# Optimization experiments

Hardware: AMD Instinct MI355X
Metric: run time of the kernel (lower is better)

The kernel has to match this reference:

```python
import jax, jax.numpy as jnp
import numpy as np

HIDDEN = 4096
INTER = 11008
GROUPSIZE = 128
PACK = 8


def dequant_gptq(qweight, scales, zeros, groupsize):
    """Dequantize GPTQ 4-bit packed weights.
    qweight: [K//8, N] int32 (8 nibbles along K), scales: [G, N] fp16,
    zeros: [G, N//8] int32 (8 nibbles along N). Returns [K, N] float32:
    w[k,n] = q[k,n]*s[g,n] - (z[g,n]+1)*s[g,n],  g = k // groupsize.
    """
    K = qweight.shape[0] * PACK
    N = qweight.shape[1]
    k = jnp.arange(K)
    # unpack along K: [K, N]
    q = (qweight[k // PACK, :] >> ((k % PACK) * 4)[:, None]) & 15
    n = jnp.arange(N)
    # unpack zero-points along N: [G, N]
    z = (zeros[:, n // PACK] >> ((n % PACK) * 4)[None, :]) & 15
    s = scales.astype(jnp.float32)                       # [G, N]
    zp = (z.astype(jnp.float32) + 1.0) * s               # [G, N]
    g = k // groupsize
    return q.astype(jnp.float32) * s[g] - zp[g]          # [K, N]


def setup_inputs() -> dict:
    key = jax.random.key(0)
    ks = jax.random.split(key, 11)
    imax = 2147483647
    G_h = HIDDEN // GROUPSIZE      # 32
    G_i = (INTER + GROUPSIZE - 1) // GROUPSIZE  # 86
    x = (jax.random.normal(ks[0], (2, 2048, HIDDEN), dtype=jnp.float32) * 0.5).astype(jnp.float16)
    return {
        "x": x,
        "gate_qweight": jax.random.randint(ks[1], (HIDDEN // PACK, INTER), 0, imax, dtype=jnp.int32),
        "gate_scales": (jax.random.uniform(ks[2], (G_h, INTER), dtype=jnp.float32) * 0.01 + 0.001).astype(jnp.float16),
        "gate_zeros": jax.random.randint(ks[3], (G_h, INTER // PACK), 0, imax, dtype=jnp.int32),
        "up_qweight": jax.random.randint(ks[4], (HIDDEN // PACK, INTER), 0, imax, dtype=jnp.int32),
        "up_scales": (jax.random.uniform(ks[5], (G_h, INTER), dtype=jnp.float32) * 0.01 + 0.001).astype(jnp.float16),
        "up_zeros": jax.random.randint(ks[6], (G_h, INTER // PACK), 0, imax, dtype=jnp.int32),
        "down_qweight": jax.random.randint(ks[7], (INTER // PACK, HIDDEN), 0, imax, dtype=jnp.int32),
        "down_scales": (jax.random.uniform(ks[8], (G_i, HIDDEN), dtype=jnp.float32) * 0.01 + 0.001).astype(jnp.float16),
        "down_zeros": jax.random.randint(ks[9], (G_i, HIDDEN // PACK), 0, imax, dtype=jnp.int32),
    }


def reference(x, gate_qweight, gate_scales, gate_zeros,
              up_qweight, up_scales, up_zeros,
              down_qweight, down_scales, down_zeros):
    B, S, H = x.shape
    x2 = x.reshape(-1, H).astype(jnp.float32)            # [M, H]
    Wg = dequant_gptq(gate_qweight, gate_scales, gate_zeros, GROUPSIZE)  # [H, I]
    Wu = dequant_gptq(up_qweight, up_scales, up_zeros, GROUPSIZE)        # [H, I]
    Wd = dequant_gptq(down_qweight, down_scales, down_zeros, GROUPSIZE)  # [I, H]
    gate = x2 @ Wg                                       # [M, I] fp32 accumulate
    up = x2 @ Wu                                         # [M, I]
    inter = gate * jax.nn.sigmoid(gate) * up             # SiLU(gate) * up
    out = (inter @ Wd).astype(jnp.float16)               # [M, H]
    return out.reshape(B, S, H)
```

## Files before the change

### kernel.cpp

```cpp
#include <hip/hip_runtime.h>
#include <stdint.h>


#define HIDDEN 4096
#define INTER  11008
#define BM 256
#define BN 256
#define BK 64

typedef __bf16 bf16x8 __attribute__((ext_vector_type(8)));
typedef float f32x4 __attribute__((ext_vector_type(4)));

__device__ __forceinline__ ushort f2bf_rne(float f) {
  uint32_t u = __float_as_uint(f);
  u += 0x7FFFu + ((u >> 16) & 1u);
  return (ushort)(u >> 16);
}

__device__ __forceinline__ float bf2f(ushort h) {
  return __uint_as_float(((uint32_t)h) << 16);
}

__global__ void f32_to_bf16_kernel(const float* __restrict__ src,
                                   ushort* __restrict__ dst, int n4) {
  const int i = blockIdx.x * 256 + threadIdx.x;
  if (i < n4) {
    const float4 v = ((const float4*)src)[i];
    ushort4 o;
    o.x = f2bf_rne(v.x); o.y = f2bf_rne(v.y);
    o.z = f2bf_rne(v.z); o.w = f2bf_rne(v.w);
    ((ushort4*)dst)[i] = o;
  }
}

__global__ void dequant_kernel(const int32_t* __restrict__ qw,
                               const float* __restrict__ sc,
                               const int32_t* __restrict__ zr,
                               ushort* __restrict__ Bp,
                               int Nfull, int n0, int nc) {
  const int n_local = blockIdx.x * 128 + threadIdx.x;
  const int k8 = blockIdx.y;
  const int n = n0 + n_local;
  const int g = k8 >> 4;
  const uint32_t q = (uint32_t)qw[(size_t)k8 * Nfull + n];
  const float s = sc[(size_t)g * Nfull + n];
  const uint32_t zv = (uint32_t)zr[(size_t)g * (Nfull >> 3) + (n >> 3)];
  const int z1 = (int)((zv >> ((n & 7) * 4)) & 15u) + 1;
  union { ushort h[8]; uint4 v; } o;
#pragma unroll
  for (int j = 0; j < 8; j++) {
    const int qi = (int)((q >> (4 * j)) & 15u) - z1;
    o.h[j] = f2bf_rne((float)qi * s);
  }
  *(uint4*)(Bp + ((size_t)k8 * nc + n_local) * 8) = o.v;
}

#define GL_LDS(gp, lp)                                                        \
  __builtin_amdgcn_global_load_lds(                                           \
      (const __attribute__((address_space(1))) uint32_t*)(gp),                \
      (__attribute__((address_space(3))) uint32_t*)(lp), 16, 0, 0)
#define BAR()  do { __builtin_amdgcn_s_barrier(); asm volatile("" ::: "memory"); } while (0)
#define WVM4() asm volatile("s_waitcnt vmcnt(4)" ::: "memory")
#define WVM0() asm volatile("s_waitcnt vmcnt(0)" ::: "memory")
#define WLG0() asm volatile("s_waitcnt lgkmcnt(0)" ::: "memory")

template <int MODE>
__launch_bounds__(512, 2)
__global__ void gemm_bt_kernel(const ushort* __restrict__ A,
                               const ushort* __restrict__ Bp,
                               void* __restrict__ Cv,
                               int K, int nc, int lda, int ldc) {
  __shared__ ushort sAs[2][BM * BK];
  __shared__ ushort sBs[2][(BK / 8) * BN * 8];

  const int tid = threadIdx.x;
  const int w = tid >> 6;
  const int lane = tid & 63;
  const int l16 = lane & 15;
  const int quad = lane >> 4;
  const int wm16 = (w >> 2) * 16;
  const int wn = (w & 3) * 64;

  const int gx = gridDim.x;
  const int nwg = gx * (int)gridDim.y;
  const int orig = blockIdx.y * gx + blockIdx.x;
  const int q8 = nwg >> 3, r8 = nwg & 7;
  const int xcd = orig & 7, sidx = orig >> 3;
  const int wg = (xcd < r8 ? xcd * (q8 + 1) : r8 * (q8 + 1) + (xcd - r8) * q8) + sidx;
  const int m0 = (wg / gx) * BM;
  const int bn0 = (wg % gx) * BN;

  const int arow = tid >> 3;
  const int apk8 = ((tid & 7) ^ (arow & 7)) * 8;
  const int bpr = tid >> 8;
  const int bcol = tid & 255;
  const ushort* aSrc = A + (size_t)(m0 + arow) * lda + apk8;
  const ushort* bSrc = Bp + ((size_t)bpr * nc + bn0 + bcol) * 8;

  f32x4 acc[8][4];
#pragma unroll
  for (int a = 0; a < 8; a++)
#pragma unroll
    for (int j = 0; j < 4; j++) acc[a][j] = (f32x4){0.f, 0.f, 0.f, 0.f};

  const int NT = K / BK;

#define STAGE_A(r, buf, kt) \
  GL_LDS(aSrc + (size_t)(r) * 64 * lda + (kt), (buf) + (r) * 4096 + w * 512)
#define STAGE_B(r, buf, kp) \
  GL_LDS(bSrc + ((kp) + (size_t)(r) * 2) * (size_t)nc * 8, (buf) + (r) * 4096 + w * 512)

  {
    ushort* sAn = sAs[0];
    ushort* sBn = sBs[0];
    STAGE_A(0, sAn, (size_t)0); STAGE_A(1, sAn, (size_t)0);
    STAGE_B(0, sBn, (size_t)0); STAGE_B(1, sBn, (size_t)0);
    STAGE_A(2, sAn, (size_t)0); STAGE_A(3, sAn, (size_t)0);
    STAGE_B(2, sBn, (size_t)0); STAGE_B(3, sBn, (size_t)0);
  }

#pragma unroll 1
  for (int t = 0; t < NT; ++t) {
    const ushort* sAc = sAs[t & 1];
    const ushort* sBc = sBs[t & 1];
    ushort* sAn = sAs[(t & 1) ^ 1];
    ushort* sBn = sBs[(t & 1) ^ 1];
    const int tn = (t + 1 < NT) ? t + 1 : t;
    const size_t ktn = (size_t)tn * BK;
    const size_t kpn = (size_t)tn * 8;

    WVM4(); BAR();

    bf16x8 af[4], bf[4];
    const ushort* pA0 = sAc + (size_t)(wm16 + l16) * 64 + ((quad ^ (l16 & 7)) * 8);
    const ushort* pA1 = sAc + (size_t)(wm16 + l16) * 64 + (((4 ^ quad) ^ (l16 & 7)) * 8);
    const ushort* pB0 = sBc + ((size_t)(quad * 256) + wn + l16) * 8;
    const ushort* pB1 = sBc + ((size_t)((4 + quad) * 256) + wn + l16) * 8;

#pragma unroll
    for (int i = 0; i < 4; i++) af[i] = *(const bf16x8*)(pA0 + i * 2048);
#pragma unroll
    for (int j = 0; j < 4; j++) bf[j] = *(const bf16x8*)(pB0 + j * 128);
    STAGE_A(0, sAn, ktn); STAGE_A(1, sAn, ktn);
    BAR(); WLG0();
    __builtin_amdgcn_s_setprio(1);
#pragma unroll
    for (int i = 0; i < 4; i++)
#pragma unroll
      for (int j = 0; j < 4; j++)
        acc[i][j] = __builtin_amdgcn_mfma_f32_16x16x32_bf16(af[i], bf[j], acc[i][j], 0, 0, 0);
    __builtin_amdgcn_s_setprio(0);
    WVM4();
    BAR();

#pragma unroll
    for (int i = 0; i < 4; i++) af[i] = *(const bf16x8*)(pA0 + 128 * 64 + i * 2048);
    STAGE_B(0, sBn, kpn); STAGE_B(1, sBn, kpn);
    BAR(); WLG0();
    __builtin_amdgcn_s_setprio(1);
#pragma unroll
    for (int i = 0; i < 4; i++)
#pragma unroll
      for (int j = 0; j < 4; j++)
        acc[4 + i][j] = __builtin_amdgcn_mfma_f32_16x16x32_bf16(af[i], bf[j], acc[4 + i][j], 0, 0, 0);
    __builtin_amdgcn_s_setprio(0);
    WVM4();
    BAR();

#pragma unroll
    for (int i = 0; i < 4; i++) af[i] = *(const bf16x8*)(pA1 + i * 2048);
#pragma unroll
    for (int j = 0; j < 4; j++) bf[j] = *(const bf16x8*)(pB1 + j * 128);
    STAGE_A(2, sAn, ktn); STAGE_A(3, sAn, ktn);
    BAR(); WLG0();
    __builtin_amdgcn_s_setprio(1);
#pragma unroll
    for (int i = 0; i < 4; i++)
#pragma unroll
      for (int j = 0; j < 4; j++)
        acc[i][j] = __builtin_amdgcn_mfma_f32_16x16x32_bf16(af[i], bf[j], acc[i][j], 0, 0, 0);
    __builtin_amdgcn_s_setprio(0);
    BAR();

#pragma unroll
    for (int i = 0; i < 4; i++) af[i] = *(const bf16x8*)(pA1 + 128 * 64 + i * 2048);
    STAGE_B(2, sBn, kpn); STAGE_B(3, sBn, kpn);
    BAR(); WLG0();
    __builtin_amdgcn_s_setprio(1);
#pragma unroll
    for (int i = 0; i < 4; i++)
#pragma unroll
      for (int j = 0; j < 4; j++)
        acc[4 + i][j] = __builtin_amdgcn_mfma_f32_16x16x32_bf16(af[i], bf[j], acc[4 + i][j], 0, 0, 0);
    __builtin_amdgcn_s_setprio(0);
  }
  WVM0();

#pragma unroll
  for (int a = 0; a < 8; a++) {
    const int gmb = m0 + (a >> 2) * 128 + (a & 3) * 32 + wm16 + quad * 4;
#pragma unroll
    for (int r = 0; r < 4; r++) {
      const int gm = gmb + r;
      if (MODE == 2) {
        float* crow = (float*)Cv + (size_t)gm * ldc + bn0 + wn;
#pragma unroll
        for (int j = 0; j < 4; j++) crow[j * 16 + l16] = acc[a][j][r];
      } else {
        ushort* crow = (ushort*)Cv + (size_t)gm * ldc + bn0 + wn;
#pragma unroll
        for (int j = 0; j < 4; j++) {
          float v = acc[a][j][r];
          if (MODE == 1) {
            const float gv = bf2f(crow[j * 16 + l16]);
            v = (gv / (1.0f + __expf(-gv))) * v;
          }
          crow[j * 16 + l16] = f2bf_rne(v);
        }
      }
    }
  }
}

extern "C" void kernel_launch(void* const* d_in, const int* in_sizes, int n_in,
                              void* d_out, int out_size, void* d_ws, size_t ws_size,
                              hipStream_t stream) {
  (void)n_in; (void)out_size;
  const float*   x   = (const float*)d_in[0];
  const int32_t* gq  = (const int32_t*)d_in[1];
  const float*   gs  = (const float*)d_in[2];
  const int32_t* gz  = (const int32_t*)d_in[3];
  const int32_t* uq  = (const int32_t*)d_in[4];
  const float*   us  = (const float*)d_in[5];
  const int32_t* uz  = (const int32_t*)d_in[6];
  const int32_t* dq  = (const int32_t*)d_in[7];
  const float*   dsc = (const float*)d_in[8];
  const int32_t* dz  = (const int32_t*)d_in[9];
  float* outp = (float*)d_out;

  const int M = in_sizes[0] / HIDDEN;

  const size_t W = ws_size;
  const size_t col12 = (size_t)HIDDEN * 2;
  const size_t col3  = (size_t)INTER * 2;
  const size_t xb_bytes = (size_t)M * HIDDEN * 2;
  int MC = 256;
  for (int cand = M; cand >= 256; cand >>= 1) {
    if (xb_bytes + (size_t)cand * INTER * 2 + col3 * 256 <= W) { MC = cand; break; }
  }
  ushort* xb = (ushort*)d_ws;
  ushort* gi = xb + (size_t)M * HIDDEN;
  ushort* wb = gi + (size_t)MC * INTER;
  const size_t used = xb_bytes + (size_t)MC * INTER * 2;
  const size_t wbuf = (W > used) ? W - used : 0;
  int NC12 = (int)(wbuf / col12); NC12 &= ~255;
  if (NC12 < 256) NC12 = 256;
  if (NC12 > INTER) NC12 = INTER;
  int NC3 = (int)(wbuf / col3); NC3 &= ~255;
  if (NC3 < 256) NC3 = 256;
  if (NC3 > HIDDEN) NC3 = HIDDEN;

  const int n4 = M * HIDDEN / 4;
  f32_to_bf16_kernel<<<(n4 + 255) / 256, 256, 0, stream>>>(x, xb, n4);

  for (int m0 = 0; m0 < M; m0 += MC) {
    const ushort* xm = xb + (size_t)m0 * HIDDEN;
    for (int n0 = 0; n0 < INTER; ) {
      int nc = INTER - n0; if (nc > NC12) nc = NC12;
      dequant_kernel<<<dim3(nc / 128, HIDDEN / 8), 128, 0, stream>>>(
          gq, gs, gz, wb, INTER, n0, nc);
      gemm_bt_kernel<0><<<dim3(nc / BN, MC / BM), 512, 0, stream>>>(
          xm, wb, gi + n0, HIDDEN, nc, HIDDEN, INTER);
      n0 += nc;
    }
    for (int n0 = 0; n0 < INTER; ) {
      int nc = INTER - n0; if (nc > NC12) nc = NC12;
      dequant_kernel<<<dim3(nc / 128, HIDDEN / 8), 128, 0, stream>>>(
          uq, us, uz, wb, INTER, n0, nc);
      gemm_bt_kernel<1><<<dim3(nc / BN, MC / BM), 512, 0, stream>>>(
          xm, wb, gi + n0, HIDDEN, nc, HIDDEN, INTER);
      n0 += nc;
    }
    for (int n0 = 0; n0 < HIDDEN; ) {
      int nc = HIDDEN - n0; if (nc > NC3) nc = NC3;
      dequant_kernel<<<dim3(nc / 128, INTER / 8), 128, 0, stream>>>(
          dq, dsc, dz, wb, HIDDEN, n0, nc);
      gemm_bt_kernel<2><<<dim3(nc / BN, MC / BM), 512, 0, stream>>>(
          gi, wb, (void*)(outp + (size_t)m0 * HIDDEN + n0), INTER, nc, INTER, HIDDEN);
      n0 += nc;
    }
  }
}
```

Measured before the change: 1.165 ms.

## Double-buffer register fragments to overlap LDS reads with MFMA in GEMM main loop

Restructures the GEMM main loop so the next phase's A/B fragments are read from LDS into a second register set while the current MFMA block runs. The first fragments of the next tile are prefetched at the end of each iteration, and waits are relaxed from vmcnt(4) to vmcnt(2) with fewer barriers. sched_barrier fences stop the compiler from reordering loads around the MFMA blocks. This is meant to hide LDS latency behind tensor-core work, at the cost of more fragment registers and a trickier ordering of barriers and waitcnts, which could race on the buffers.

```diff
diff --git a/kernel.cpp b/kernel.cpp
--- a/kernel.cpp
+++ b/kernel.cpp
@@ -61,8 +61,10 @@
       (__attribute__((address_space(3))) uint32_t*)(lp), 16, 0, 0)
 #define BAR()  do { __builtin_amdgcn_s_barrier(); asm volatile("" ::: "memory"); } while (0)
 #define WVM4() asm volatile("s_waitcnt vmcnt(4)" ::: "memory")
+#define WVM2() asm volatile("s_waitcnt vmcnt(2)" ::: "memory")
 #define WVM0() asm volatile("s_waitcnt vmcnt(0)" ::: "memory")
 #define WLG0() asm volatile("s_waitcnt lgkmcnt(0)" ::: "memory")
+#define SCHED0() __builtin_amdgcn_sched_barrier(0)
 
 template <int MODE>
 __launch_bounds__(512, 2)
@@ -80,6 +82,7 @@
   const int quad = lane >> 4;
   const int wm16 = (w >> 2) * 16;
   const int wn = (w & 3) * 64;
+  const int swz = l16 & 7;
 
   const int gx = gridDim.x;
   const int nwg = gx * (int)gridDim.y;
@@ -103,6 +106,8 @@
 #pragma unroll
     for (int j = 0; j < 4; j++) acc[a][j] = (f32x4){0.f, 0.f, 0.f, 0.f};
 
+  bf16x8 afs0[4], afs1[4], bfs0[4], bfs1[4];
+
   const int NT = K / BK;
 
 #define STAGE_A(r, buf, kt) \
@@ -111,12 +116,21 @@
   GL_LDS(bSrc + ((kp) + (size_t)(r) * 2) * (size_t)nc * 8, (buf) + (r) * 4096 + w * 512)
 
   {
-    ushort* sAn = sAs[0];
-    ushort* sBn = sBs[0];
-    STAGE_A(0, sAn, (size_t)0); STAGE_A(1, sAn, (size_t)0);
-    STAGE_B(0, sBn, (size_t)0); STAGE_B(1, sBn, (size_t)0);
-    STAGE_A(2, sAn, (size_t)0); STAGE_A(3, sAn, (size_t)0);
-    STAGE_B(2, sBn, (size_t)0); STAGE_B(3, sBn, (size_t)0);
+    ushort* sA0 = sAs[0];
+    ushort* sB0 = sBs[0];
+    STAGE_A(0, sA0, (size_t)0); STAGE_A(1, sA0, (size_t)0);
+    STAGE_B(0, sB0, (size_t)0); STAGE_B(1, sB0, (size_t)0);
+    STAGE_A(2, sA0, (size_t)0); STAGE_A(3, sA0, (size_t)0);
+    STAGE_B(2, sB0, (size_t)0); STAGE_B(3, sB0, (size_t)0);
+    WVM4();
+    BAR();
+    const ushort* a0 = sA0 + (size_t)(wm16 + l16) * 64;
+#pragma unroll
+    for (int i = 0; i < 4; i++)
+      afs0[i] = *(const bf16x8*)(a0 + i * 2048 + ((quad ^ swz) * 8));
+#pragma unroll
+    for (int j = 0; j < 4; j++)
+      bfs0[j] = *(const bf16x8*)(sB0 + ((size_t)(quad * 256) + wn + j * 16 + l16) * 8);
   }
 
 #pragma unroll 1
@@ -128,70 +142,75 @@
     const int tn = (t + 1 < NT) ? t + 1 : t;
     const size_t ktn = (size_t)tn * BK;
     const size_t kpn = (size_t)tn * 8;
-
-    WVM4(); BAR();
-
-    bf16x8 af[4], bf[4];
-    const ushort* pA0 = sAc + (size_t)(wm16 + l16) * 64 + ((quad ^ (l16 & 7)) * 8);
-    const ushort* pA1 = sAc + (size_t)(wm16 + l16) * 64 + (((4 ^ quad) ^ (l16 & 7)) * 8);
-    const ushort* pB0 = sBc + ((size_t)(quad * 256) + wn + l16) * 8;
-    const ushort* pB1 = sBc + ((size_t)((4 + quad) * 256) + wn + l16) * 8;
-
-#pragma unroll
-    for (int i = 0; i < 4; i++) af[i] = *(const bf16x8*)(pA0 + i * 2048);
-#pragma unroll
-    for (int j = 0; j < 4; j++) bf[j] = *(const bf16x8*)(pB0 + j * 128);
+    const ushort* aLo = sAc + (size_t)(wm16 + l16) * 64;
+    const ushort* aHi = aLo + 128 * 64;
+
+    WVM2();
+    BAR(); WLG0(); SCHED0();
+#pragma unroll
+    for (int i = 0; i < 4; i++)
+      afs1[i] = *(const bf16x8*)(aHi + i * 2048 + ((quad ^ swz) * 8));
     STAGE_A(0, sAn, ktn); STAGE_A(1, sAn, ktn);
-    BAR(); WLG0();
+    SCHED0();
     __builtin_amdgcn_s_setprio(1);
 #pragma unroll
     for (int i = 0; i < 4; i++)
 #pragma unroll
       for (int j = 0; j < 4; j++)
-        acc[i][j] = __builtin_amdgcn_mfma_f32_16x16x32_bf16(af[i], bf[j], acc[i][j], 0, 0, 0);
+        acc[i][j] = __builtin_amdgcn_mfma_f32_16x16x32_bf16(afs0[i], bfs0[j], acc[i][j], 0, 0, 0);
     __builtin_amdgcn_s_setprio(0);
-    WVM4();
-    BAR();
-
-#pragma unroll
-    for (int i = 0; i < 4; i++) af[i] = *(const bf16x8*)(pA0 + 128 * 64 + i * 2048);
+
+    WVM2();
+    BAR(); WLG0(); SCHED0();
+#pragma unroll
+    for (int i = 0; i < 4; i++)
+      afs0[i] = *(const bf16x8*)(aLo + i * 2048 + (((4 ^ quad) ^ swz) * 8));
+#pragma unroll
+    for (int j = 0; j < 4; j++)
+      bfs1[j] = *(const bf16x8*)(sBc + ((size_t)((4 + quad) * 256) + wn + j * 16 + l16) * 8);
     STAGE_B(0, sBn, kpn); STAGE_B(1, sBn, kpn);
-    BAR(); WLG0();
+    SCHED0();
     __builtin_amdgcn_s_setprio(1);
 #pragma unroll
     for (int i = 0; i < 4; i++)
 #pragma unroll
       for (int j = 0; j < 4; j++)
-        acc[4 + i][j] = __builtin_amdgcn_mfma_f32_16x16x32_bf16(af[i], bf[j], acc[4 + i][j], 0, 0, 0);
+        acc[4 + i][j] = __builtin_amdgcn_mfma_f32_16x16x32_bf16(afs1[i], bfs0[j], acc[4 + i][j], 0, 0, 0);
     __builtin_amdgcn_s_setprio(0);
-    WVM4();
-    BAR();
-
-#pragma unroll
-    for (int i = 0; i < 4; i++) af[i] = *(const bf16x8*)(pA1 + i * 2048);
-#pragma unroll
-    for (int j = 0; j < 4; j++) bf[j] = *(const bf16x8*)(pB1 + j * 128);
+
+    BAR(); WLG0(); SCHED0();
+#pragma unroll
+    for (int i = 0; i < 4; i++)
+      afs1[i] = *(const bf16x8*)(aHi + i * 2048 + (((4 ^ quad) ^ swz) * 8));
     STAGE_A(2, sAn, ktn); STAGE_A(3, sAn, ktn);
-    BAR(); WLG0();
+    SCHED0();
     __builtin_amdgcn_s_setprio(1);
 #pragma unroll
     for (int i = 0; i < 4; i++)
 #pragma unroll
       for (int j = 0; j < 4; j++)
-        acc[i][j] = __builtin_amdgcn_mfma_f32_16x16x32_bf16(af[i], bf[j], acc[i][j], 0, 0, 0);
+        acc[i][j] = __builtin_amdgcn_mfma_f32_16x16x32_bf16(afs0[i], bfs1[j], acc[i][j], 0, 0, 0);
     __builtin_amdgcn_s_setprio(0);
-    BAR();
-
-#pragma unroll
-    for (int i = 0; i < 4; i++) af[i] = *(const bf16x8*)(pA1 + 128 * 64 + i * 2048);
+
+    WVM2();
+    BAR(); WLG0(); SCHED0();
+    {
+      const ushort* aNx = sAn + (size_t)(wm16 + l16) * 64;
+#pragma unroll
+      for (int i = 0; i < 4; i++)
+        afs0[i] = *(const bf16x8*)(aNx + i * 2048 + ((quad ^ swz) * 8));
+#pragma unroll
+      for (int j = 0; j < 4; j++)
+        bfs0[j] = *(const bf16x8*)(sBn + ((size_t)(quad * 256) + wn + j * 16 + l16) * 8);
+    }
     STAGE_B(2, sBn, kpn); STAGE_B(3, sBn, kpn);
-    BAR(); WLG0();
+    SCHED0();
     __builtin_amdgcn_s_setprio(1);
 #pragma unroll
     for (int i = 0; i < 4; i++)
 #pragma unroll
       for (int j = 0; j < 4; j++)
-        acc[4 + i][j] = __builtin_amdgcn_mfma_f32_16x16x32_bf16(af[i], bf[j], acc[4 + i][j], 0, 0, 0);
+        acc[4 + i][j] = __builtin_amdgcn_mfma_f32_16x16x32_bf16(afs1[i], bfs1[j], acc[4 + i][j], 0, 0, 0);
     __builtin_amdgcn_s_setprio(0);
   }
   WVM0();
```

Result: slower. 1.383 ms (+18.7%).

## Restructure GEMM main loop into quadrant-based 8-phase ping-pong schedule

Applied to the files above, without the earlier changes.

Replaces the 4-phase per-K-tile loop with a two-tile unrolled loop. Each 8-wave block now owns a contiguous 128x64 quadrant per wave, split into 2x2 subtiles, and issues interleaved LDS reads, MFMA and global-to-LDS staging with fewer lgkmcnt waits and a vmcnt(6) depth. The intent is to keep loads in flight longer and improve A/B fragment reuse across MFMA clusters, reducing stalls at barriers. The cost is more register pressure from extra fragment buffers and a more intricate staging order that assumes NT is even.

```diff
diff --git a/kernel.cpp b/kernel.cpp
--- a/kernel.cpp
+++ b/kernel.cpp
@@ -60,9 +60,8 @@
       (const __attribute__((address_space(1))) uint32_t*)(gp),                \
       (__attribute__((address_space(3))) uint32_t*)(lp), 16, 0, 0)
 #define BAR()  do { __builtin_amdgcn_s_barrier(); asm volatile("" ::: "memory"); } while (0)
-#define WVM4() asm volatile("s_waitcnt vmcnt(4)" ::: "memory")
+#define WVM6() asm volatile("s_waitcnt vmcnt(6)" ::: "memory")
 #define WVM0() asm volatile("s_waitcnt vmcnt(0)" ::: "memory")
-#define WLG0() asm volatile("s_waitcnt lgkmcnt(0)" ::: "memory")
 
 template <int MODE>
 __launch_bounds__(512, 2)
@@ -70,16 +69,19 @@
                                const ushort* __restrict__ Bp,
                                void* __restrict__ Cv,
                                int K, int nc, int lda, int ldc) {
-  __shared__ ushort sAs[2][BM * BK];
-  __shared__ ushort sBs[2][(BK / 8) * BN * 8];
+  __shared__ ushort sA0[BM * BK];
+  __shared__ ushort sB0[(BK / 8) * BN * 8];
+  __shared__ ushort sA1[BM * BK];
+  __shared__ ushort sB1[(BK / 8) * BN * 8];
 
   const int tid = threadIdx.x;
   const int w = tid >> 6;
   const int lane = tid & 63;
   const int l16 = lane & 15;
   const int quad = lane >> 4;
-  const int wm16 = (w >> 2) * 16;
-  const int wn = (w & 3) * 64;
+  const int wm = w >> 2;
+  const int wn = w & 3;
+  const int swz = l16 & 7;
 
   const int gx = gridDim.x;
   const int nwg = gx * (int)gridDim.y;
@@ -97,125 +99,145 @@
   const ushort* aSrc = A + (size_t)(m0 + arow) * lda + apk8;
   const ushort* bSrc = Bp + ((size_t)bpr * nc + bn0 + bcol) * 8;
 
-  f32x4 acc[8][4];
-#pragma unroll
-  for (int a = 0; a < 8; a++)
-#pragma unroll
-    for (int j = 0; j < 4; j++) acc[a][j] = (f32x4){0.f, 0.f, 0.f, 0.f};
+  f32x4 acc[2][2][4][2];
+#pragma unroll
+  for (int rh = 0; rh < 2; rh++)
+#pragma unroll
+    for (int ch = 0; ch < 2; ch++)
+#pragma unroll
+      for (int i = 0; i < 4; i++)
+#pragma unroll
+        for (int jj = 0; jj < 2; jj++)
+          acc[rh][ch][i][jj] = (f32x4){0.f, 0.f, 0.f, 0.f};
+
+  bf16x8 afr[4][2], bA[2][2], bB[2][2];
 
   const int NT = K / BK;
-
-#define STAGE_A(r, buf, kt) \
-  GL_LDS(aSrc + (size_t)(r) * 64 * lda + (kt), (buf) + (r) * 4096 + w * 512)
-#define STAGE_B(r, buf, kp) \
-  GL_LDS(bSrc + ((kp) + (size_t)(r) * 2) * (size_t)nc * 8, (buf) + (r) * 4096 + w * 512)
-
-  {
-    ushort* sAn = sAs[0];
-    ushort* sBn = sBs[0];
-    STAGE_A(0, sAn, (size_t)0); STAGE_A(1, sAn, (size_t)0);
-    STAGE_B(0, sBn, (size_t)0); STAGE_B(1, sBn, (size_t)0);
-    STAGE_A(2, sAn, (size_t)0); STAGE_A(3, sAn, (size_t)0);
-    STAGE_B(2, sBn, (size_t)0); STAGE_B(3, sBn, (size_t)0);
-  }
+  const int NI = NT >> 1;
+
+#define SA(r, s, buf) \
+  GL_LDS(aSrc + (size_t)(r) * 64 * lda + (size_t)(s) * BK, (buf) + (r) * 4096 + w * 512)
+#define SB(r, s, buf) \
+  GL_LDS(bSrc + ((size_t)(s) * 8 + (r) * 2) * (size_t)nc * 8, (buf) + (r) * 4096 + w * 512)
+
+#define RD_A(sbuf, rh)                                                         \
+  do {                                                                         \
+    const ushort* _a = (sbuf) + ((size_t)(wm * 128 + (rh) * 64 + l16)) * 64;   \
+    _Pragma("unroll") for (int i = 0; i < 4; i++) {                            \
+      afr[i][0] = *(const bf16x8*)(_a + i * 1024 + ((quad ^ swz) * 8));        \
+      afr[i][1] = *(const bf16x8*)(_a + i * 1024 + (((quad + 4) ^ swz) * 8));  \
+    }                                                                          \
+  } while (0)
+#define RD_B(sbuf, ch, dst)                                                    \
+  do {                                                                         \
+    const int _c = wn * 64 + (ch) * 32 + l16;                                  \
+    _Pragma("unroll") for (int jj = 0; jj < 2; jj++) {                         \
+      dst[jj][0] = *(const bf16x8*)((sbuf) + ((quad * 256) + _c + jj * 16) * 8);       \
+      dst[jj][1] = *(const bf16x8*)((sbuf) + (((quad + 4) * 256) + _c + jj * 16) * 8); \
+    }                                                                          \
+  } while (0)
+#define MM(rh, ch, bset)                                                       \
+  do {                                                                         \
+    __builtin_amdgcn_s_setprio(1);                                             \
+    _Pragma("unroll") for (int kk = 0; kk < 2; kk++)                           \
+    _Pragma("unroll") for (int i = 0; i < 4; i++)                              \
+    _Pragma("unroll") for (int jj = 0; jj < 2; jj++)                           \
+      acc[rh][ch][i][jj] = __builtin_amdgcn_mfma_f32_16x16x32_bf16(            \
+          afr[i][kk], bset[jj][kk], acc[rh][ch][i][jj], 0, 0, 0);              \
+    __builtin_amdgcn_s_setprio(0);                                             \
+  } while (0)
+
+  SA(0, 0, sA0); SA(2, 0, sA0);
+  SB(0, 0, sB0); SB(1, 0, sB0); SB(2, 0, sB0); SB(3, 0, sB0);
+  SA(1, 0, sA0); SA(3, 0, sA0);
+  SA(0, 1, sA1); SA(2, 1, sA1);
+  SB(0, 1, sB1); SB(1, 1, sB1); SB(2, 1, sB1); SB(3, 1, sB1);
+  WVM6();
+  BAR();
 
 #pragma unroll 1
-  for (int t = 0; t < NT; ++t) {
-    const ushort* sAc = sAs[t & 1];
-    const ushort* sBc = sBs[t & 1];
-    ushort* sAn = sAs[(t & 1) ^ 1];
-    ushort* sBn = sBs[(t & 1) ^ 1];
-    const int tn = (t + 1 < NT) ? t + 1 : t;
-    const size_t ktn = (size_t)tn * BK;
-    const size_t kpn = (size_t)tn * 8;
-
-    WVM4(); BAR();
-
-    bf16x8 af[4], bf[4];
-    const ushort* pA0 = sAc + (size_t)(wm16 + l16) * 64 + ((quad ^ (l16 & 7)) * 8);
-    const ushort* pA1 = sAc + (size_t)(wm16 + l16) * 64 + (((4 ^ quad) ^ (l16 & 7)) * 8);
-    const ushort* pB0 = sBc + ((size_t)(quad * 256) + wn + l16) * 8;
-    const ushort* pB1 = sBc + ((size_t)((4 + quad) * 256) + wn + l16) * 8;
-
-#pragma unroll
-    for (int i = 0; i < 4; i++) af[i] = *(const bf16x8*)(pA0 + i * 2048);
-#pragma unroll
-    for (int j = 0; j < 4; j++) bf[j] = *(const bf16x8*)(pB0 + j * 128);
-    STAGE_A(0, sAn, ktn); STAGE_A(1, sAn, ktn);
-    BAR(); WLG0();
-    __builtin_amdgcn_s_setprio(1);
-#pragma unroll
-    for (int i = 0; i < 4; i++)
-#pragma unroll
-      for (int j = 0; j < 4; j++)
-        acc[i][j] = __builtin_amdgcn_mfma_f32_16x16x32_bf16(af[i], bf[j], acc[i][j], 0, 0, 0);
-    __builtin_amdgcn_s_setprio(0);
-    WVM4();
-    BAR();
-
-#pragma unroll
-    for (int i = 0; i < 4; i++) af[i] = *(const bf16x8*)(pA0 + 128 * 64 + i * 2048);
-    STAGE_B(0, sBn, kpn); STAGE_B(1, sBn, kpn);
-    BAR(); WLG0();
-    __builtin_amdgcn_s_setprio(1);
-#pragma unroll
-    for (int i = 0; i < 4; i++)
-#pragma unroll
-      for (int j = 0; j < 4; j++)
-        acc[4 + i][j] = __builtin_amdgcn_mfma_f32_16x16x32_bf16(af[i], bf[j], acc[4 + i][j], 0, 0, 0);
-    __builtin_amdgcn_s_setprio(0);
-    WVM4();
-    BAR();
-
-#pragma unroll
-    for (int i = 0; i < 4; i++) af[i] = *(const bf16x8*)(pA1 + i * 2048);
-#pragma unroll
-    for (int j = 0; j < 4; j++) bf[j] = *(const bf16x8*)(pB1 + j * 128);
-    STAGE_A(2, sAn, ktn); STAGE_A(3, sAn, ktn);
-    BAR(); WLG0();
-    __builtin_amdgcn_s_setprio(1);
-#pragma unroll
-    for (int i = 0; i < 4; i++)
-#pragma unroll
-      for (int j = 0; j < 4; j++)
-        acc[i][j] = __builtin_amdgcn_mfma_f32_16x16x32_bf16(af[i], bf[j], acc[i][j], 0, 0, 0);
-    __builtin_amdgcn_s_setprio(0);
-    BAR();
-
-#pragma unroll
-    for (int i = 0; i < 4; i++) af[i] = *(const bf16x8*)(pA1 + 128 * 64 + i * 2048);
-    STAGE_B(2, sBn, kpn); STAGE_B(3, sBn, kpn);
-    BAR(); WLG0();
-    __builtin_amdgcn_s_setprio(1);
-#pragma unroll
-    for (int i = 0; i < 4; i++)
-#pragma unroll
-      for (int j = 0; j < 4; j++)
-        acc[4 + i][j] = __builtin_amdgcn_mfma_f32_16x16x32_bf16(af[i], bf[j], acc[4 + i][j], 0, 0, 0);
-    __builtin_amdgcn_s_setprio(0);
+  for (int it = 0; it < NI; ++it) {
+    const int c1 = 2 * it + 1;
+    const int s2 = (2 * it + 2 < NT) ? 2 * it + 2 : NT - 2;
+    const int s3 = (2 * it + 3 < NT) ? 2 * it + 3 : NT - 1;
+
+    RD_A(sA0, 0); RD_B(sB0, 0, bA);
+    SA(1, c1, sA1); SA(3, c1, sA1);
+    BAR();
+    MM(0, 0, bA);
+    BAR();
+    RD_B(sB0, 1, bB);
+    SA(0, s2, sA0); SA(2, s2, sA0);
+    BAR();
+    MM(0, 1, bB);
+    BAR();
+    RD_A(sA0, 1);
+    SB(0, s2, sB0); SB(1, s2, sB0);
+    BAR();
+    MM(1, 0, bA);
+    BAR();
+    SB(2, s2, sB0); SB(3, s2, sB0);
+    BAR();
+    MM(1, 1, bB);
+    WVM6();
+    BAR();
+    RD_A(sA1, 0); RD_B(sB1, 0, bA);
+    SA(1, s2, sA0); SA(3, s2, sA0);
+    BAR();
+    MM(0, 0, bA);
+    BAR();
+    RD_B(sB1, 1, bB);
+    SA(0, s3, sA1); SA(2, s3, sA1);
+    BAR();
+    MM(0, 1, bB);
+    BAR();
+    RD_A(sA1, 1);
+    SB(0, s3, sB1); SB(1, s3, sB1);
+    BAR();
+    MM(1, 0, bA);
+    BAR();
+    SB(2, s3, sB1); SB(3, s3, sB1);
+    BAR();
+    MM(1, 1, bB);
+    WVM6();
+    BAR();
   }
   WVM0();
 
-#pragma unroll
-  for (int a = 0; a < 8; a++) {
-    const int gmb = m0 + (a >> 2) * 128 + (a & 3) * 32 + wm16 + quad * 4;
-#pragma unroll
-    for (int r = 0; r < 4; r++) {
-      const int gm = gmb + r;
-      if (MODE == 2) {
-        float* crow = (float*)Cv + (size_t)gm * ldc + bn0 + wn;
-#pragma unroll
-        for (int j = 0; j < 4; j++) crow[j * 16 + l16] = acc[a][j][r];
-      } else {
-        ushort* crow = (ushort*)Cv + (size_t)gm * ldc + bn0 + wn;
-#pragma unroll
-        for (int j = 0; j < 4; j++) {
-          float v = acc[a][j][r];
-          if (MODE == 1) {
-            const float gv = bf2f(crow[j * 16 + l16]);
-            v = (gv / (1.0f + __expf(-gv))) * v;
-          }
-          crow[j * 16 + l16] = f2bf_rne(v);
+#undef SA
+#undef SB
+#undef RD_A
+#undef RD_B
+#undef MM
+
+#pragma unroll
+  for (int rh = 0; rh < 2; rh++) {
+#pragma unroll
+    for (int i = 0; i < 4; i++) {
+#pragma unroll
+      for (int r = 0; r < 4; r++) {
+        const int gm = m0 + wm * 128 + rh * 64 + i * 16 + quad * 4 + r;
+        if (MODE == 2) {
+          float* crow = (float*)Cv + (size_t)gm * ldc + bn0 + wn * 64;
+#pragma unroll
+          for (int ch = 0; ch < 2; ch++)
+#pragma unroll
+            for (int jj = 0; jj < 2; jj++)
+              crow[ch * 32 + jj * 16 + l16] = acc[rh][ch][i][jj][r];
+        } else {
+          ushort* crow = (ushort*)Cv + (size_t)gm * ldc + bn0 + wn * 64;
+#pragma unroll
+          for (int ch = 0; ch < 2; ch++)
+#pragma unroll
+            for (int jj = 0; jj < 2; jj++) {
+              float v = acc[rh][ch][i][jj][r];
+              const int cn = ch * 32 + jj * 16 + l16;
+              if (MODE == 1) {
+                const float gv = bf2f(crow[cn]);
+                v = (gv / (1.0f + __expf(-gv))) * v;
+              }
+              crow[cn] = f2bf_rne(v);
+            }
         }
       }
     }
```

Result: slower. 1.373 ms (+17.8%).

## Fuse GPTQ dequantization into GEMM B-tile staging, dropping separate dequant pass

Applied to the files above, without the earlier changes.

Removes the standalone dequant kernel and the bf16 weight buffer. Each GEMM workgroup now loads packed int4 weights, scales and zeros straight into registers, expands them to bf16 with packed converts and FMA, and writes them to LDS inside the pipelined main loop. This avoids writing and re-reading the full dequantized weights in global memory and the extra launches. In exchange, every M-block redoes the dequant arithmetic and the B loads become synchronous register loads rather than async global-to-LDS copies, which could stall the MFMA pipeline.

```diff
diff --git a/kernel.cpp b/kernel.cpp
--- a/kernel.cpp
+++ b/kernel.cpp
@@ -33,28 +33,6 @@
   }
 }
 
-__global__ void dequant_kernel(const int32_t* __restrict__ qw,
-                               const float* __restrict__ sc,
-                               const int32_t* __restrict__ zr,
-                               ushort* __restrict__ Bp,
-                               int Nfull, int n0, int nc) {
-  const int n_local = blockIdx.x * 128 + threadIdx.x;
-  const int k8 = blockIdx.y;
-  const int n = n0 + n_local;
-  const int g = k8 >> 4;
-  const uint32_t q = (uint32_t)qw[(size_t)k8 * Nfull + n];
-  const float s = sc[(size_t)g * Nfull + n];
-  const uint32_t zv = (uint32_t)zr[(size_t)g * (Nfull >> 3) + (n >> 3)];
-  const int z1 = (int)((zv >> ((n & 7) * 4)) & 15u) + 1;
-  union { ushort h[8]; uint4 v; } o;
-#pragma unroll
-  for (int j = 0; j < 8; j++) {
-    const int qi = (int)((q >> (4 * j)) & 15u) - z1;
-    o.h[j] = f2bf_rne((float)qi * s);
-  }
-  *(uint4*)(Bp + ((size_t)k8 * nc + n_local) * 8) = o.v;
-}
-
 #define GL_LDS(gp, lp)                                                        \
   __builtin_amdgcn_global_load_lds(                                           \
       (const __attribute__((address_space(1))) uint32_t*)(gp),                \
@@ -64,12 +42,34 @@
 #define WVM0() asm volatile("s_waitcnt vmcnt(0)" ::: "memory")
 #define WLG0() asm volatile("s_waitcnt lgkmcnt(0)" ::: "memory")
 
+__device__ __forceinline__ uint4 expand_packet(uint32_t v, float s, float nz1s) {
+  const uint32_t lo = v & 0x0F0F0F0Fu;
+  const uint32_t hi = (v >> 4) & 0x0F0F0F0Fu;
+  uint4 o;
+  float a0, a1;
+  a0 = fmaf((float)(lo & 0xFFu), s, nz1s);
+  a1 = fmaf((float)(hi & 0xFFu), s, nz1s);
+  asm("v_cvt_pk_bf16_f32 %0, %1, %2" : "=v"(o.x) : "v"(a0), "v"(a1));
+  a0 = fmaf((float)((lo >> 8) & 0xFFu), s, nz1s);
+  a1 = fmaf((float)((hi >> 8) & 0xFFu), s, nz1s);
+  asm("v_cvt_pk_bf16_f32 %0, %1, %2" : "=v"(o.y) : "v"(a0), "v"(a1));
+  a0 = fmaf((float)((lo >> 16) & 0xFFu), s, nz1s);
+  a1 = fmaf((float)((hi >> 16) & 0xFFu), s, nz1s);
+  asm("v_cvt_pk_bf16_f32 %0, %1, %2" : "=v"(o.z) : "v"(a0), "v"(a1));
+  a0 = fmaf((float)(lo >> 24), s, nz1s);
+  a1 = fmaf((float)(hi >> 24), s, nz1s);
+  asm("v_cvt_pk_bf16_f32 %0, %1, %2" : "=v"(o.w) : "v"(a0), "v"(a1));
+  return o;
+}
+
 template <int MODE>
 __launch_bounds__(512, 2)
-__global__ void gemm_bt_kernel(const ushort* __restrict__ A,
-                               const ushort* __restrict__ Bp,
-                               void* __restrict__ Cv,
-                               int K, int nc, int lda, int ldc) {
+__global__ void gemm_fused_kernel(const ushort* __restrict__ A,
+                                  const int32_t* __restrict__ qw,
+                                  const float* __restrict__ sc,
+                                  const int32_t* __restrict__ zr,
+                                  void* __restrict__ Cv,
+                                  int K, int Nfull, int lda, int ldc) {
   __shared__ ushort sAs[2][BM * BK];
   __shared__ ushort sBs[2][(BK / 8) * BN * 8];
 
@@ -80,6 +80,7 @@
   const int quad = lane >> 4;
   const int wm16 = (w >> 2) * 16;
   const int wn = (w & 3) * 64;
+  const int swz = l16 & 7;
 
   const int gx = gridDim.x;
   const int nwg = gx * (int)gridDim.y;
@@ -92,10 +93,14 @@
 
   const int arow = tid >> 3;
   const int apk8 = ((tid & 7) ^ (arow & 7)) * 8;
-  const int bpr = tid >> 8;
+  const ushort* aSrc = A + (size_t)(m0 + arow) * lda + apk8;
+
   const int bcol = tid & 255;
-  const ushort* aSrc = A + (size_t)(m0 + arow) * lda + apk8;
-  const ushort* bSrc = Bp + ((size_t)bpr * nc + bn0 + bcol) * 8;
+  const int prg = tid >> 8;
+  const int32_t* qcol = qw + bn0 + bcol;
+  const float* scol = sc + bn0 + bcol;
+  const int32_t* zcol = zr + ((bn0 + bcol) >> 3);
+  const int zsh = (bcol & 7) * 4;
 
   f32x4 acc[8][4];
 #pragma unroll
@@ -107,19 +112,47 @@
 
 #define STAGE_A(r, buf, kt) \
   GL_LDS(aSrc + (size_t)(r) * 64 * lda + (kt), (buf) + (r) * 4096 + w * 512)
-#define STAGE_B(r, buf, kp) \
-  GL_LDS(bSrc + ((kp) + (size_t)(r) * 2) * (size_t)nc * 8, (buf) + (r) * 4096 + w * 512)
-
-  {
-    ushort* sAn = sAs[0];
-    ushort* sBn = sBs[0];
-    STAGE_A(0, sAn, (size_t)0); STAGE_A(1, sAn, (size_t)0);
-    STAGE_B(0, sBn, (size_t)0); STAGE_B(1, sBn, (size_t)0);
-    STAGE_A(2, sAn, (size_t)0); STAGE_A(3, sAn, (size_t)0);
-    STAGE_B(2, sBn, (size_t)0); STAGE_B(3, sBn, (size_t)0);
-  }
-
-#pragma unroll 1
+
+  uint32_t b4[4]; float sNx; uint32_t zNx;
+#define LOADB(s)                                                   \
+  do {                                                             \
+    const size_t rb = (size_t)(s) * 8 + prg;                       \
+    b4[0] = (uint32_t)qcol[(rb + 0) * (size_t)Nfull];              \
+    b4[1] = (uint32_t)qcol[(rb + 2) * (size_t)Nfull];              \
+    b4[2] = (uint32_t)qcol[(rb + 4) * (size_t)Nfull];              \
+    b4[3] = (uint32_t)qcol[(rb + 6) * (size_t)Nfull];              \
+    sNx = scol[(size_t)((s) >> 1) * Nfull];                        \
+    zNx = (uint32_t)zcol[(size_t)((s) >> 1) * (Nfull >> 3)];       \
+  } while (0)
+
+#define EXPB(buf)                                                        \
+  do {                                                                   \
+    const int z1 = (int)((zNx >> zsh) & 15u) + 1;                        \
+    const float nz = -((float)z1 * sNx);                                 \
+    _Pragma("unroll") for (int r = 0; r < 4; r++) {                      \
+      const uint4 pk = expand_packet(b4[r], sNx, nz);                    \
+      *(uint4*)((buf) + ((size_t)(prg + 2 * r) * 256 + bcol) * 8) = pk;  \
+    }                                                                    \
+  } while (0)
+
+#define MM16(base)                                                       \
+  do {                                                                   \
+    __builtin_amdgcn_s_setprio(1);                                       \
+    _Pragma("unroll") for (int i = 0; i < 4; i++)                        \
+    _Pragma("unroll") for (int j = 0; j < 4; j++)                        \
+      acc[(base) + i][j] = __builtin_amdgcn_mfma_f32_16x16x32_bf16(      \
+          af[i], bf[j], acc[(base) + i][j], 0, 0, 0);                    \
+    __builtin_amdgcn_s_setprio(0);                                       \
+  } while (0)
+
+  LOADB(0);
+  STAGE_A(0, sAs[0], (size_t)0); STAGE_A(1, sAs[0], (size_t)0);
+  STAGE_A(2, sAs[0], (size_t)0); STAGE_A(3, sAs[0], (size_t)0);
+  WVM4();
+  EXPB(sBs[0]);
+  WVM0(); WLG0();
+  BAR();
+
   for (int t = 0; t < NT; ++t) {
     const ushort* sAc = sAs[t & 1];
     const ushort* sBc = sBs[t & 1];
@@ -127,74 +160,52 @@
     ushort* sBn = sBs[(t & 1) ^ 1];
     const int tn = (t + 1 < NT) ? t + 1 : t;
     const size_t ktn = (size_t)tn * BK;
-    const size_t kpn = (size_t)tn * 8;
-
-    WVM4(); BAR();
 
     bf16x8 af[4], bf[4];
-    const ushort* pA0 = sAc + (size_t)(wm16 + l16) * 64 + ((quad ^ (l16 & 7)) * 8);
-    const ushort* pA1 = sAc + (size_t)(wm16 + l16) * 64 + (((4 ^ quad) ^ (l16 & 7)) * 8);
-    const ushort* pB0 = sBc + ((size_t)(quad * 256) + wn + l16) * 8;
-    const ushort* pB1 = sBc + ((size_t)((4 + quad) * 256) + wn + l16) * 8;
+    const ushort* pA0 = sAc + (size_t)(wm16 + l16) * 64 + ((quad ^ swz) * 8);
+    const ushort* pA1 = sAc + (size_t)(wm16 + l16) * 64 + (((4 ^ quad) ^ swz) * 8);
 
 #pragma unroll
     for (int i = 0; i < 4; i++) af[i] = *(const bf16x8*)(pA0 + i * 2048);
 #pragma unroll
-    for (int j = 0; j < 4; j++) bf[j] = *(const bf16x8*)(pB0 + j * 128);
+    for (int j = 0; j < 4; j++)
+      bf[j] = *(const bf16x8*)(sBc + ((size_t)(quad * 256) + wn + j * 16 + l16) * 8);
+    LOADB(tn);
+    BAR(); WLG0();
+    MM16(0);
+    BAR();
+
+#pragma unroll
+    for (int i = 0; i < 4; i++) af[i] = *(const bf16x8*)(pA0 + 128 * 64 + i * 2048);
     STAGE_A(0, sAn, ktn); STAGE_A(1, sAn, ktn);
     BAR(); WLG0();
-    __builtin_amdgcn_s_setprio(1);
-#pragma unroll
-    for (int i = 0; i < 4; i++)
-#pragma unroll
-      for (int j = 0; j < 4; j++)
-        acc[i][j] = __builtin_amdgcn_mfma_f32_16x16x32_bf16(af[i], bf[j], acc[i][j], 0, 0, 0);
-    __builtin_amdgcn_s_setprio(0);
+    MM16(4);
+    BAR();
+
+#pragma unroll
+    for (int i = 0; i < 4; i++) af[i] = *(const bf16x8*)(pA1 + i * 2048);
+#pragma unroll
+    for (int j = 0; j < 4; j++)
+      bf[j] = *(const bf16x8*)(sBc + ((size_t)((4 + quad) * 256) + wn + j * 16 + l16) * 8);
+    STAGE_A(2, sAn, ktn); STAGE_A(3, sAn, ktn);
+    BAR(); WLG0();
+    MM16(0);
     WVM4();
     BAR();
 
 #pragma unroll
-    for (int i = 0; i < 4; i++) af[i] = *(const bf16x8*)(pA0 + 128 * 64 + i * 2048);
-    STAGE_B(0, sBn, kpn); STAGE_B(1, sBn, kpn);
-    BAR(); WLG0();
-    __builtin_amdgcn_s_setprio(1);
-#pragma unroll
-    for (int i = 0; i < 4; i++)
-#pragma unroll
-      for (int j = 0; j < 4; j++)
-        acc[4 + i][j] = __builtin_amdgcn_mfma_f32_16x16x32_bf16(af[i], bf[j], acc[4 + i][j], 0, 0, 0);
-    __builtin_amdgcn_s_setprio(0);
-    WVM4();
-    BAR();
-
-#pragma unroll
-    for (int i = 0; i < 4; i++) af[i] = *(const bf16x8*)(pA1 + i * 2048);
-#pragma unroll
-    for (int j = 0; j < 4; j++) bf[j] = *(const bf16x8*)(pB1 + j * 128);
-    STAGE_A(2, sAn, ktn); STAGE_A(3, sAn, ktn);
-    BAR(); WLG0();
-    __builtin_amdgcn_s_setprio(1);
-#pragma unroll
-    for (int i = 0; i < 4; i++)
-#pragma unroll
-      for (int j = 0; j < 4; j++)
-        acc[i][j] = __builtin_amdgcn_mfma_f32_16x16x32_bf16(af[i], bf[j], acc[i][j], 0, 0, 0);
-    __builtin_amdgcn_s_setprio(0);
-    BAR();
-
-#pragma unroll
     for (int i = 0; i < 4; i++) af[i] = *(const bf16x8*)(pA1 + 128 * 64 + i * 2048);
-    STAGE_B(2, sBn, kpn); STAGE_B(3, sBn, kpn);
-    BAR(); WLG0();
-    __builtin_amdgcn_s_setprio(1);
-#pragma unroll
-    for (int i = 0; i < 4; i++)
-#pragma unroll
-      for (int j = 0; j < 4; j++)
-        acc[4 + i][j] = __builtin_amdgcn_mfma_f32_16x16x32_bf16(af[i], bf[j], acc[4 + i][j], 0, 0, 0);
-    __builtin_amdgcn_s_setprio(0);
-  }
-  WVM0();
+    EXPB(sBn);
+    BAR(); WLG0();
+    MM16(4);
+    WVM0();
+    BAR();
+  }
+
+#undef STAGE_A
+#undef LOADB
+#undef EXPB
+#undef MM16
 
 #pragma unroll
   for (int a = 0; a < 8; a++) {
@@ -211,11 +222,12 @@
 #pragma unroll
         for (int j = 0; j < 4; j++) {
           float v = acc[a][j][r];
+          const int cn = j * 16 + l16;
           if (MODE == 1) {
-            const float gv = bf2f(crow[j * 16 + l16]);
+            const float gv = bf2f(crow[cn]);
             v = (gv / (1.0f + __expf(-gv))) * v;
           }
-          crow[j * 16 + l16] = f2bf_rne(v);
+          crow[cn] = f2bf_rne(v);
         }
       }
     }
@@ -241,53 +253,24 @@
   const int M = in_sizes[0] / HIDDEN;
 
   const size_t W = ws_size;
-  const size_t col12 = (size_t)HIDDEN * 2;
-  const size_t col3  = (size_t)INTER * 2;
   const size_t xb_bytes = (size_t)M * HIDDEN * 2;
   int MC = 256;
   for (int cand = M; cand >= 256; cand >>= 1) {
-    if (xb_bytes + (size_t)cand * INTER * 2 + col3 * 256 <= W) { MC = cand; break; }
+    if (xb_bytes + (size_t)cand * INTER * 2 <= W) { MC = cand; break; }
   }
   ushort* xb = (ushort*)d_ws;
   ushort* gi = xb + (size_t)M * HIDDEN;
-  ushort* wb = gi + (size_t)MC * INTER;
-  const size_t used = xb_bytes + (size_t)MC * INTER * 2;
-  const size_t wbuf = (W > used) ? W - used : 0;
-  int NC12 = (int)(wbuf / col12); NC12 &= ~255;
-  if (NC12 < 256) NC12 = 256;
-  if (NC12 > INTER) NC12 = INTER;
-  int NC3 = (int)(wbuf / col3); NC3 &= ~255;
-  if (NC3 < 256) NC3 = 256;
-  if (NC3 > HIDDEN) NC3 = HIDDEN;
 
   const int n4 = M * HIDDEN / 4;
   f32_to_bf16_kernel<<<(n4 + 255) / 256, 256, 0, stream>>>(x, xb, n4);
 
   for (int m0 = 0; m0 < M; m0 += MC) {
     const ushort* xm = xb + (size_t)m0 * HIDDEN;
-    for (int n0 = 0; n0 < INTER; ) {
-      int nc = INTER - n0; if (nc > NC12) nc = NC12;
-      dequant_kernel<<<dim3(nc / 128, HIDDEN / 8), 128, 0, stream>>>(
-          gq, gs, gz, wb, INTER, n0, nc);
-      gemm_bt_kernel<0><<<dim3(nc / BN, MC / BM), 512, 0, stream>>>(
-          xm, wb, gi + n0, HIDDEN, nc, HIDDEN, INTER);
-      n0 += nc;
-    }
-    for (int n0 = 0; n0 < INTER; ) {
-      int nc = INTER - n0; if (nc > NC12) nc = NC12;
-      dequant_kernel<<<dim3(nc / 128, HIDDEN / 8), 128, 0, stream>>>(
-          uq, us, uz, wb, INTER, n0, nc);
-      gemm_bt_kernel<1><<<dim3(nc / BN, MC / BM), 512, 0, stream>>>(
-          xm, wb, gi + n0, HIDDEN, nc, HIDDEN, INTER);
-      n0 += nc;
-    }
-    for (int n0 = 0; n0 < HIDDEN; ) {
-      int nc = HIDDEN - n0; if (nc > NC3) nc = NC3;
-      dequant_kernel<<<dim3(nc / 128, INTER / 8), 128, 0, stream>>>(
-          dq, dsc, dz, wb, HIDDEN, n0, nc);
-      gemm_bt_kernel<2><<<dim3(nc / BN, MC / BM), 512, 0, stream>>>(
-          gi, wb, (void*)(outp + (size_t)m0 * HIDDEN + n0), INTER, nc, INTER, HIDDEN);
-      n0 += nc;
-    }
-  }
-}
+    gemm_fused_kernel<0><<<dim3(INTER / BN, MC / BM), 512, 0, stream>>>(
+        xm, gq, gs, gz, gi, HIDDEN, INTER, HIDDEN, INTER);
+    gemm_fused_kernel<1><<<dim3(INTER / BN, MC / BM), 512, 0, stream>>>(
+        xm, uq, us, uz, gi, HIDDEN, INTER, HIDDEN, INTER);
+    gemm_fused_kernel<2><<<dim3(HIDDEN / BN, MC / BM), 512, 0, stream>>>(
+        gi, dq, dsc, dz, (void*)(outp + (size_t)m0 * HIDDEN), INTER, HIDDEN, INTER, HIDDEN);
+  }
+}
```

Measured after the change: 1.467 ms. +25.9%, slower.
